# Performance work log

Hardware: AMD Instinct MI355X
Metric: run time of the kernel (lower is better)

The kernel has to match this reference:

```python
import jax, jax.numpy as jnp
import numpy as np


def setup_inputs() -> dict:
    key = jax.random.key(0)
    k1, k2, k3 = jax.random.split(key, 3)
    B, S, D_IN, D_OUT = 2, 2048, 4096, 4096
    x = jax.random.normal(k1, (B, S, D_IN), dtype=jnp.float32)
    # int8 quantized weight (stored as int32 container, values in int8 range)
    weight = jax.random.randint(k2, (D_OUT, D_IN), 0, 127, dtype=jnp.int32)
    weight_scaler = jax.random.uniform(k3, (D_OUT,), dtype=jnp.float32)
    return {"x": x, "weight": weight, "weight_scaler": weight_scaler}


def reference(x, weight, weight_scaler):
    # Dequantize per-output-channel: w_fp = int8_weight * scaler[:, None]
    w = weight.astype(jnp.float32) * weight_scaler[:, None]  # [O, I]
    # F.linear: x @ w.T
    return jnp.einsum("bsi,oi->bso", x, w)
```

## Files before the change

### kernel.cpp

```cpp
#include <hip/hip_runtime.h>

typedef int i32x4 __attribute__((ext_vector_type(4)));

#define AS1 __attribute__((address_space(1)))
#define AS3 __attribute__((address_space(3)))

__global__ __launch_bounds__(256) void quant_kernel(
    const float4* __restrict__ x, const int4* __restrict__ w,
    signed char* __restrict__ xq, signed char* __restrict__ wq,
    float* __restrict__ sx, int M, int Kq) {
  const int tid = threadIdx.x;
  if ((int)blockIdx.x < M) {
    const int r = blockIdx.x;
    float4 v[4];
    #pragma unroll
    for (int j = 0; j < 4; ++j) v[j] = x[(size_t)r * 1024 + tid * 4 + j];
    float m = 0.f;
    #pragma unroll
    for (int j = 0; j < 4; ++j)
      m = fmaxf(m, fmaxf(fmaxf(fabsf(v[j].x), fabsf(v[j].y)),
                         fmaxf(fabsf(v[j].z), fabsf(v[j].w))));
    #pragma unroll
    for (int off = 1; off < 64; off <<= 1) m = fmaxf(m, __shfl_xor(m, off));
    __shared__ float wmax[4];
    if ((tid & 63) == 0) wmax[tid >> 6] = m;
    __syncthreads();
    m = fmaxf(fmaxf(wmax[0], wmax[1]), fmaxf(wmax[2], wmax[3]));
    const float inv = (m > 0.f) ? 127.0f / m : 0.f;
    if (tid == 0) sx[r] = m * (1.0f / 127.0f);
    signed char q[16];
    #pragma unroll
    for (int j = 0; j < 4; ++j) {
      q[j * 4 + 0] = (signed char)__float2int_rn(v[j].x * inv);
      q[j * 4 + 1] = (signed char)__float2int_rn(v[j].y * inv);
      q[j * 4 + 2] = (signed char)__float2int_rn(v[j].z * inv);
      q[j * 4 + 3] = (signed char)__float2int_rn(v[j].w * inv);
    }
    ((int4*)xq)[(size_t)r * 256 + tid] = *(const int4*)q;
  } else {
    const int b = blockIdx.x - M;
    int4 v[4];
    #pragma unroll
    for (int j = 0; j < 4; ++j) v[j] = w[(size_t)b * 1024 + tid * 4 + j];
    signed char q[16];
    #pragma unroll
    for (int j = 0; j < 4; ++j) {
      q[j * 4 + 0] = (signed char)v[j].x; q[j * 4 + 1] = (signed char)v[j].y;
      q[j * 4 + 2] = (signed char)v[j].z; q[j * 4 + 3] = (signed char)v[j].w;
    }
    ((int4*)wq)[(size_t)b * 256 + tid] = *(const int4*)q;
  }
}

__global__ __launch_bounds__(256, 2) void gemm_i8_kernel(
    const signed char* __restrict__ A,
    const signed char* __restrict__ B,
    const float* __restrict__ sx,
    const float* __restrict__ scaler,
    float* __restrict__ C,
    int M, int N, int K)
{
  __shared__ signed char sA[3][256 * 64];
  __shared__ signed char sB[3][128 * 64];

  const int tid  = threadIdx.x;
  const int wave = tid >> 6;
  const int lane = tid & 63;
  const int bm = blockIdx.y << 8;
  const int bn = blockIdx.x << 7;

  const int wm = (wave >> 1) << 7;
  const int wn = (wave & 1) << 6;
  const int l15  = lane & 15;
  const int quad = lane >> 4;

  const int srow = tid >> 2;
  const int kg = (tid & 3) ^ ((srow >> 1) & 3);
  const signed char* ga = A + (size_t)(bm + srow) * K + kg * 16;
  const signed char* gb = B + (size_t)(bn + srow) * K + kg * 16;
  const size_t rstep = (size_t)64 * K;
  const int ldst = tid * 16;

  const int pk   = (quad ^ ((l15 >> 1) & 3)) << 4;
  const int aoff = (wm + l15) * 64 + pk;
  const int boff = (wn + l15) * 64 + pk;

  i32x4 acc[8][4] = {};

#define STAGE(tt, sb) do { const size_t ko_ = (size_t)(tt) * 64;             \
    __builtin_amdgcn_global_load_lds((AS1 void*)(ga + ko_),             (AS3 void*)(&sA[sb][ldst]),         16, 0, 0); \
    __builtin_amdgcn_global_load_lds((AS1 void*)(ga + ko_ + rstep),     (AS3 void*)(&sA[sb][4096 + ldst]),  16, 0, 0); \
    __builtin_amdgcn_global_load_lds((AS1 void*)(ga + ko_ + 2 * rstep), (AS3 void*)(&sA[sb][8192 + ldst]),  16, 0, 0); \
    __builtin_amdgcn_global_load_lds((AS1 void*)(ga + ko_ + 3 * rstep), (AS3 void*)(&sA[sb][12288 + ldst]), 16, 0, 0); \
    __builtin_amdgcn_global_load_lds((AS1 void*)(gb + ko_),             (AS3 void*)(&sB[sb][ldst]),         16, 0, 0); \
    __builtin_amdgcn_global_load_lds((AS1 void*)(gb + ko_ + rstep),     (AS3 void*)(&sB[sb][4096 + ldst]),  16, 0, 0); } while (0)

  const int nt = K >> 6;

  STAGE(0, 0); STAGE(1, 1);
  asm volatile("s_waitcnt vmcnt(6)" ::: "memory");
  __builtin_amdgcn_s_barrier();
  __builtin_amdgcn_sched_barrier(0);

  int br = 0;
  int bs = 2;
  for (int t = 0; t < nt; ++t) {
    const signed char* la = sA[br];
    const signed char* lb = sB[br];

    if (t < nt - 2) STAGE(t + 2, bs);

    i32x4 av[8], bv[4];
    #pragma unroll
    for (int ni = 0; ni < 4; ++ni) bv[ni] = *(const i32x4*)&lb[boff + ni * 1024];
    #pragma unroll
    for (int mi = 0; mi < 8; ++mi) av[mi] = *(const i32x4*)&la[aoff + mi * 1024];

    __builtin_amdgcn_s_setprio(1);
    #pragma unroll
    for (int mi = 0; mi < 8; ++mi)
      #pragma unroll
      for (int ni = 0; ni < 4; ++ni)
        acc[mi][ni] = __builtin_amdgcn_mfma_i32_16x16x64_i8(av[mi], bv[ni], acc[mi][ni], 0, 0, 0);
    __builtin_amdgcn_s_setprio(0);

    if (t < nt - 2)        asm volatile("s_waitcnt vmcnt(6)" ::: "memory");
    else if (t == nt - 2)  asm volatile("s_waitcnt vmcnt(0)" ::: "memory");
    if (t < nt - 1) {
      __builtin_amdgcn_s_barrier();
      __builtin_amdgcn_sched_barrier(0);
    }
    br = (br == 2) ? 0 : br + 1;
    bs = (bs == 2) ? 0 : bs + 1;
  }
#undef STAGE

  #pragma unroll
  for (int mi = 0; mi < 8; ++mi) {
    const int gm0 = bm + wm + mi * 16 + quad * 4;
    float sr[4];
    #pragma unroll
    for (int r = 0; r < 4; ++r) sr[r] = sx[gm0 + r];
    #pragma unroll
    for (int ni = 0; ni < 4; ++ni) {
      const int gn = bn + wn + ni * 16 + l15;
      const float sc = scaler[gn];
      #pragma unroll
      for (int r = 0; r < 4; ++r)
        C[(size_t)(gm0 + r) * N + gn] = (float)acc[mi][ni][r] * sr[r] * sc;
    }
  }
}

extern "C" void kernel_launch(void* const* d_in, const int* in_sizes, int n_in,
                              void* d_out, int out_size, void* d_ws, size_t ws_size,
                              hipStream_t stream) {
  const float* x  = (const float*)d_in[0];
  const int*   w  = (const int*)d_in[1];
  const float* sc = (const float*)d_in[2];
  float* out = (float*)d_out;

  const int N = in_sizes[2];
  const int K = in_sizes[1] / N;
  const int M = in_sizes[0] / K;

  signed char* Aq = (signed char*)d_ws;
  signed char* Bq = Aq + (size_t)M * K;
  float* sx = (float*)(Bq + (size_t)N * K);

  const int wBlocks = (N * K) / (256 * 16);
  quant_kernel<<<M + wBlocks, 256, 0, stream>>>(
      (const float4*)x, (const int4*)w, Aq, Bq, sx, M, K / 16);

  dim3 grid(N / 128, M / 256);
  gemm_i8_kernel<<<grid, 256, 0, stream>>>(Aq, Bq, sx, sc, out, M, N, K);
}
```

Measured before the change: 241.9 us.

## Switch int8 GEMM to 32x32x32 MFMA and coalesce quantization stores

The GEMM inner loop now uses the 32x32x32 int8 MFMA instead of 16x16x64. Each wave computes its 128x64 tile as 4x2 blocks of 32x32, with two k-substeps per 64-wide LDS tile, and the operand reads and epilogue indexing are remapped to match. Larger MFMA tiles need fewer LDS operand reads per MAC and fewer instructions. The quantization kernel now has threads read and write interleaved 4-element chunks with packed 32-bit stores, giving coalesced accesses instead of per-thread 16-byte strided chunks.

```diff
diff --git a/kernel.cpp b/kernel.cpp
--- a/kernel.cpp
+++ b/kernel.cpp
@@ -1,6 +1,7 @@
 #include <hip/hip_runtime.h>
 
-typedef int i32x4 __attribute__((ext_vector_type(4)));
+typedef int i32x4  __attribute__((ext_vector_type(4)));
+typedef int i32x16 __attribute__((ext_vector_type(16)));
 
 #define AS1 __attribute__((address_space(1)))
 #define AS3 __attribute__((address_space(3)))
@@ -14,7 +15,7 @@
     const int r = blockIdx.x;
     float4 v[4];
     #pragma unroll
-    for (int j = 0; j < 4; ++j) v[j] = x[(size_t)r * 1024 + tid * 4 + j];
+    for (int j = 0; j < 4; ++j) v[j] = x[(size_t)r * 1024 + j * 256 + tid];
     float m = 0.f;
     #pragma unroll
     for (int j = 0; j < 4; ++j)
@@ -28,27 +29,25 @@
     m = fmaxf(fmaxf(wmax[0], wmax[1]), fmaxf(wmax[2], wmax[3]));
     const float inv = (m > 0.f) ? 127.0f / m : 0.f;
     if (tid == 0) sx[r] = m * (1.0f / 127.0f);
-    signed char q[16];
+    int* out = (int*)xq;
     #pragma unroll
     for (int j = 0; j < 4; ++j) {
-      q[j * 4 + 0] = (signed char)__float2int_rn(v[j].x * inv);
-      q[j * 4 + 1] = (signed char)__float2int_rn(v[j].y * inv);
-      q[j * 4 + 2] = (signed char)__float2int_rn(v[j].z * inv);
-      q[j * 4 + 3] = (signed char)__float2int_rn(v[j].w * inv);
+      const int q0 = __float2int_rn(v[j].x * inv) & 255;
+      const int q1 = __float2int_rn(v[j].y * inv) & 255;
+      const int q2 = __float2int_rn(v[j].z * inv) & 255;
+      const int q3 = __float2int_rn(v[j].w * inv) & 255;
+      out[(size_t)r * 1024 + j * 256 + tid] = q0 | (q1 << 8) | (q2 << 16) | (q3 << 24);
     }
-    ((int4*)xq)[(size_t)r * 256 + tid] = *(const int4*)q;
   } else {
     const int b = blockIdx.x - M;
     int4 v[4];
     #pragma unroll
-    for (int j = 0; j < 4; ++j) v[j] = w[(size_t)b * 1024 + tid * 4 + j];
-    signed char q[16];
+    for (int j = 0; j < 4; ++j) v[j] = w[(size_t)b * 1024 + j * 256 + tid];
+    int* out = (int*)wq;
     #pragma unroll
-    for (int j = 0; j < 4; ++j) {
-      q[j * 4 + 0] = (signed char)v[j].x; q[j * 4 + 1] = (signed char)v[j].y;
-      q[j * 4 + 2] = (signed char)v[j].z; q[j * 4 + 3] = (signed char)v[j].w;
-    }
-    ((int4*)wq)[(size_t)b * 256 + tid] = *(const int4*)q;
+    for (int j = 0; j < 4; ++j)
+      out[(size_t)b * 1024 + j * 256 + tid] =
+          (v[j].x & 255) | ((v[j].y & 255) << 8) | ((v[j].z & 255) << 16) | ((v[j].w & 255) << 24);
   }
 }
 
@@ -71,8 +70,8 @@
 
   const int wm = (wave >> 1) << 7;
   const int wn = (wave & 1) << 6;
-  const int l15  = lane & 15;
-  const int quad = lane >> 4;
+  const int l31 = lane & 31;
+  const int hi  = lane >> 5;
 
   const int srow = tid >> 2;
   const int kg = (tid & 3) ^ ((srow >> 1) & 3);
@@ -81,11 +80,13 @@
   const size_t rstep = (size_t)64 * K;
   const int ldst = tid * 16;
 
-  const int pk   = (quad ^ ((l15 >> 1) & 3)) << 4;
-  const int aoff = (wm + l15) * 64 + pk;
-  const int boff = (wn + l15) * 64 + pk;
+  const int sw  = (l31 >> 1) & 3;
+  const int pk0 = (hi ^ sw) << 4;
+  const int pk1 = ((2 | hi) ^ sw) << 4;
+  const int arow = (wm + l31) * 64;
+  const int brow = (wn + l31) * 64;
 
-  i32x4 acc[8][4] = {};
+  i32x16 acc[4][2] = {};
 
 #define STAGE(tt, sb) do { const size_t ko_ = (size_t)(tt) * 64;             \
     __builtin_amdgcn_global_load_lds((AS1 void*)(ga + ko_),             (AS3 void*)(&sA[sb][ldst]),         16, 0, 0); \
@@ -110,18 +111,26 @@
 
     if (t < nt - 2) STAGE(t + 2, bs);
 
-    i32x4 av[8], bv[4];
+    i32x4 av[4][2], bv[2][2];
     #pragma unroll
-    for (int ni = 0; ni < 4; ++ni) bv[ni] = *(const i32x4*)&lb[boff + ni * 1024];
+    for (int ni = 0; ni < 2; ++ni) {
+      bv[ni][0] = *(const i32x4*)&lb[brow + ni * 2048 + pk0];
+      bv[ni][1] = *(const i32x4*)&lb[brow + ni * 2048 + pk1];
+    }
     #pragma unroll
-    for (int mi = 0; mi < 8; ++mi) av[mi] = *(const i32x4*)&la[aoff + mi * 1024];
+    for (int mi = 0; mi < 4; ++mi) {
+      av[mi][0] = *(const i32x4*)&la[arow + mi * 2048 + pk0];
+      av[mi][1] = *(const i32x4*)&la[arow + mi * 2048 + pk1];
+    }
 
     __builtin_amdgcn_s_setprio(1);
     #pragma unroll
-    for (int mi = 0; mi < 8; ++mi)
+    for (int ks = 0; ks < 2; ++ks)
       #pragma unroll
-      for (int ni = 0; ni < 4; ++ni)
-        acc[mi][ni] = __builtin_amdgcn_mfma_i32_16x16x64_i8(av[mi], bv[ni], acc[mi][ni], 0, 0, 0);
+      for (int mi = 0; mi < 4; ++mi)
+        #pragma unroll
+        for (int ni = 0; ni < 2; ++ni)
+          acc[mi][ni] = __builtin_amdgcn_mfma_i32_32x32x32_i8(av[mi][ks], bv[ni][ks], acc[mi][ni], 0, 0, 0);
     __builtin_amdgcn_s_setprio(0);
 
     if (t < nt - 2)        asm volatile("s_waitcnt vmcnt(6)" ::: "memory");
@@ -135,19 +144,25 @@
   }
 #undef STAGE
 
+  float scn[2];
   #pragma unroll
-  for (int mi = 0; mi < 8; ++mi) {
-    const int gm0 = bm + wm + mi * 16 + quad * 4;
-    float sr[4];
+  for (int ni = 0; ni < 2; ++ni) scn[ni] = scaler[bn + wn + ni * 32 + l31];
+  #pragma unroll
+  for (int mi = 0; mi < 4; ++mi) {
+    const int gm0 = bm + wm + mi * 32 + hi * 4;
     #pragma unroll
-    for (int r = 0; r < 4; ++r) sr[r] = sx[gm0 + r];
-    #pragma unroll
-    for (int ni = 0; ni < 4; ++ni) {
-      const int gn = bn + wn + ni * 16 + l15;
-      const float sc = scaler[gn];
+    for (int rg = 0; rg < 4; ++rg) {
+      float sr[4];
       #pragma unroll
-      for (int r = 0; r < 4; ++r)
-        C[(size_t)(gm0 + r) * N + gn] = (float)acc[mi][ni][r] * sr[r] * sc;
+      for (int r = 0; r < 4; ++r) sr[r] = sx[gm0 + rg * 8 + r];
+      #pragma unroll
+      for (int ni = 0; ni < 2; ++ni) {
+        const int gn = bn + wn + ni * 32 + l31;
+        #pragma unroll
+        for (int r = 0; r < 4; ++r)
+          C[(size_t)(gm0 + rg * 8 + r) * N + gn] =
+              (float)acc[mi][ni][rg * 4 + r] * sr[r] * scn[ni];
+      }
     }
   }
 }
```

After: 246.2 us. No clear change (+1.8%).

## Coalesce quant kernel accesses and swizzle GEMM blocks across XCDs

Applied to the files above, without the earlier changes.

The quantization kernel now uses a strided per-thread layout, so consecutive threads read adjacent float4/int4 elements and write adjacent packed 32-bit words instead of 16-byte chunks 64 bytes apart. The GEMM remaps its linear block index so that blocks dispatched round-robin to the 8 XCDs get contiguous tile ranges, which should improve L2 reuse of A and B tiles. The swizzle hardcodes 8 XCDs and a 32-wide grid, so it is only valid for this problem shape (N/128 = 32, 512 blocks).

```diff
diff --git a/kernel.cpp b/kernel.cpp
--- a/kernel.cpp
+++ b/kernel.cpp
@@ -14,7 +14,7 @@
     const int r = blockIdx.x;
     float4 v[4];
     #pragma unroll
-    for (int j = 0; j < 4; ++j) v[j] = x[(size_t)r * 1024 + tid * 4 + j];
+    for (int j = 0; j < 4; ++j) v[j] = x[(size_t)r * 1024 + j * 256 + tid];
     float m = 0.f;
     #pragma unroll
     for (int j = 0; j < 4; ++j)
@@ -28,27 +28,25 @@
     m = fmaxf(fmaxf(wmax[0], wmax[1]), fmaxf(wmax[2], wmax[3]));
     const float inv = (m > 0.f) ? 127.0f / m : 0.f;
     if (tid == 0) sx[r] = m * (1.0f / 127.0f);
-    signed char q[16];
+    int* out = (int*)xq;
     #pragma unroll
     for (int j = 0; j < 4; ++j) {
-      q[j * 4 + 0] = (signed char)__float2int_rn(v[j].x * inv);
-      q[j * 4 + 1] = (signed char)__float2int_rn(v[j].y * inv);
-      q[j * 4 + 2] = (signed char)__float2int_rn(v[j].z * inv);
-      q[j * 4 + 3] = (signed char)__float2int_rn(v[j].w * inv);
+      const int q0 = __float2int_rn(v[j].x * inv) & 255;
+      const int q1 = __float2int_rn(v[j].y * inv) & 255;
+      const int q2 = __float2int_rn(v[j].z * inv) & 255;
+      const int q3 = __float2int_rn(v[j].w * inv) & 255;
+      out[(size_t)r * 1024 + j * 256 + tid] = q0 | (q1 << 8) | (q2 << 16) | (q3 << 24);
     }
-    ((int4*)xq)[(size_t)r * 256 + tid] = *(const int4*)q;
   } else {
     const int b = blockIdx.x - M;
     int4 v[4];
     #pragma unroll
-    for (int j = 0; j < 4; ++j) v[j] = w[(size_t)b * 1024 + tid * 4 + j];
-    signed char q[16];
+    for (int j = 0; j < 4; ++j) v[j] = w[(size_t)b * 1024 + j * 256 + tid];
+    int* out = (int*)wq;
     #pragma unroll
-    for (int j = 0; j < 4; ++j) {
-      q[j * 4 + 0] = (signed char)v[j].x; q[j * 4 + 1] = (signed char)v[j].y;
-      q[j * 4 + 2] = (signed char)v[j].z; q[j * 4 + 3] = (signed char)v[j].w;
-    }
-    ((int4*)wq)[(size_t)b * 256 + tid] = *(const int4*)q;
+    for (int j = 0; j < 4; ++j)
+      out[(size_t)b * 1024 + j * 256 + tid] =
+          (v[j].x & 255) | ((v[j].y & 255) << 8) | ((v[j].z & 255) << 16) | ((v[j].w & 255) << 24);
   }
 }
 
@@ -66,8 +64,13 @@
   const int tid  = threadIdx.x;
   const int wave = tid >> 6;
   const int lane = tid & 63;
-  const int bm = blockIdx.y << 8;
-  const int bn = blockIdx.x << 7;
+
+  const int lin = (int)(blockIdx.y * gridDim.x + blockIdx.x);
+  const int swz = (lin & 7) * 64 + (lin >> 3);
+  const int bxs = swz & 31;
+  const int bys = swz >> 5;
+  const int bm = bys << 8;
+  const int bn = bxs << 7;
 
   const int wm = (wave >> 1) << 7;
   const int wn = (wave & 1) << 6;
```

Measured after the change: 240.6 us. Within noise of the previous version (-0.6%).
